# Kernel optimization log

Hardware: AMD Instinct MI355X
Metric: run time of the kernel (lower is better)

Reference implementation:

```python
import jax, jax.numpy as jnp
import numpy as np

N = 50000      # nodes
E = 800000     # edges (avg degree 16)
IN, H, C = 128, 256, 47


def _linear_init(key, nin, nout):
    bound = 1.0 / np.sqrt(nin)
    kw, kb = jax.random.split(key)
    w = jax.random.uniform(kw, (nin, nout), jnp.float32, -bound, bound)
    b = jax.random.uniform(kb, (nout,), jnp.float32, -bound, bound)
    return w, b


def setup_inputs() -> dict:
    key = jax.random.key(0)
    ks = jax.random.split(key, 9)
    x = jax.random.normal(ks[0], (N, IN), jnp.float32)
    row = jax.random.randint(ks[1], (E,), 0, N)   # dst node of each edge
    col = jax.random.randint(ks[2], (E,), 0, N)   # src node of each edge
    y = jax.random.randint(ks[3], (N,), 0, C)
    train_mask = jax.random.randint(ks[4], (N,), 0, 2).astype(jnp.bool_)
    w1n, b1n = _linear_init(ks[5], IN, H)
    w1s, b1s = _linear_init(ks[6], IN, H)
    w2n, b2n = _linear_init(ks[7], H, C)
    w2s, b2s = _linear_init(ks[8], H, C)
    return {"x": x, "row": row, "col": col, "y": y, "train_mask": train_mask,
            "w1n": w1n, "b1n": b1n, "w1s": w1s, "b1s": b1s,
            "w2n": w2n, "b2n": b2n, "w2s": w2s, "b2s": b2s}


def _mean_aggr(h, row, col):
    # sparse adjacency matmul with reduce='mean': gather src feats, scatter-mean to dst
    s = jax.ops.segment_sum(h[col], row, num_segments=N)          # [N, d]
    deg = jax.ops.segment_sum(jnp.ones((E,), h.dtype), row, num_segments=N)
    return jnp.where(deg[:, None] > 0, s / jnp.maximum(deg, 1.0)[:, None], 0.0)


def reference(x, row, col, y, train_mask,
              w1n, b1n, w1s, b1s, w2n, b2n, w2s, b2s):
    # dropout in eval mode -> identity
    h = x
    # layer 1: SAGE = linear(mean_aggr(h)) + linear(h), then ReLU
    a = _mean_aggr(h, row, col)
    h1 = jax.nn.relu((a @ w1n + b1n) + (h @ w1s + b1s))           # [N, H]
    # layer 2 (output): SAGE then log_softmax
    a2 = _mean_aggr(h1, row, col)
    logits = (a2 @ w2n + b2n) + (h1 @ w2s + b2s)                  # [N, C]
    logp = jax.nn.log_softmax(logits, axis=1)
    nll = -jnp.take_along_axis(logp, y[:, None], axis=1)[:, 0]    # [N]
    m = train_mask.astype(logits.dtype)
    # nll_loss mean over train nodes; single chunk -> loss / num_chunks == loss
    loss = jnp.sum(nll * m) / jnp.maximum(jnp.sum(m), 1.0)
    return loss
```

## Files before the change

kernel.cpp:

```cpp
#include <hip/hip_runtime.h>
#include <math.h>

#define NN 50000
#define EE 800000
#define DIN 128
#define HH 256
#define CC 47
#define LK2 264
#define GS_BLOCKS 2048
#define LOSS_BLOCKS 2048

typedef short bf16x8 __attribute__((ext_vector_type(8)));
typedef float f32x4 __attribute__((ext_vector_type(4)));
typedef float f32x2 __attribute__((ext_vector_type(2)));

static __device__ __forceinline__ unsigned short f2bf(float f) {
    unsigned u = __float_as_uint(f);
    u = u + 0x7fff + ((u >> 16) & 1);
    return (unsigned short)(u >> 16);
}

__global__ __launch_bounds__(256) void prep_kernel(
    const float* __restrict__ x, const int* __restrict__ row,
    const int* __restrict__ col, const int* __restrict__ msk,
    const float* __restrict__ w1n, const float* __restrict__ w1s,
    const float* __restrict__ b1n, const float* __restrict__ b1s,
    const float* __restrict__ w2n, const float* __restrict__ w2s,
    int* __restrict__ cnt, unsigned short* __restrict__ bucket,
    unsigned* __restrict__ xq, unsigned* __restrict__ ab,
    unsigned short* __restrict__ WB1, unsigned short* __restrict__ WB2,
    float* __restrict__ bias1, unsigned* __restrict__ znq,
    int* __restrict__ mcount, int* __restrict__ mlist)
{
    int t = blockIdx.x * 256 + threadIdx.x;
    if (t < EE) {
        int r = row[t];
        int pos = atomicAdd(&cnt[r], 1);
        if (pos < 64) bucket[r * 64 + pos] = (unsigned short)col[t];
    }
    if (t < NN) {
        *(uint4*)&znq[(size_t)t * 16 + 12] = make_uint4(0u, 0u, 0u, 0u);
        int m = msk[t] ? 1 : 0;
        unsigned long long b = __ballot(m);
        int lane = threadIdx.x & 63;
        int prefix = __popcll(b & ((1ull << lane) - 1ull));
        int tot = __popcll(b);
        int base_ = 0;
        if (lane == 0 && tot) base_ = atomicAdd(mcount, tot);
        base_ = __shfl(base_, 0);
        if (m) mlist[base_ + prefix] = t;
    }
    if (t < NN * 32) {
        int i = t >> 5, c = t & 31;
        float4 v = *(const float4*)&x[(size_t)i * DIN + c * 4];
        int p = __builtin_amdgcn_cvt_pk_fp8_f32(v.x, v.y, 0, false);
        p = __builtin_amdgcn_cvt_pk_fp8_f32(v.z, v.w, p, true);
        xq[(size_t)i * 32 + c] = (unsigned)p;
        ab[(size_t)i * 128 + 64 + 2 * c]     = (unsigned)f2bf(v.x) | ((unsigned)f2bf(v.y) << 16);
        ab[(size_t)i * 128 + 64 + 2 * c + 1] = (unsigned)f2bf(v.z) | ((unsigned)f2bf(v.w) << 16);
    }
    if (t < 65536) {
        int k = t >> 8, n = t & 255;
        float v = (k < 128) ? w1n[k * HH + n] : w1s[(k - 128) * HH + n];
        WB1[n * 256 + k] = f2bf(v);
    } else if (t < 65536 + 24576) {
        int q = t - 65536;
        int k = q / 96, n = q % 96;
        float v;
        if (n < 48) v = (n < CC) ? w2n[k * CC + n] : 0.f;
        else { int m2 = n - 48; v = (m2 < CC) ? w2s[k * CC + m2] : 0.f; }
        WB2[n * 256 + k] = f2bf(v);
    } else if (t < 65536 + 24576 + 256) {
        int n = t - 65536 - 24576;
        bias1[n] = b1n[n] + b1s[n];
    }
}

__global__ __launch_bounds__(256) void agg1(const unsigned* __restrict__ xq,
                                            const int* __restrict__ cnt,
                                            const unsigned short* __restrict__ bucket,
                                            unsigned* __restrict__ ab) {
    int wave = threadIdx.x >> 6, lane = threadIdx.x & 63;
    const int h = lane >> 5, hl = lane & 31;
    const int W = gridDim.x * 4;
    for (int i = blockIdx.x * 4 + wave; i < NN; i += W) {
        int e = cnt[i];
        float dvs = fmaxf((float)e, 1.0f);
        if (e > 64) e = 64;
        float A0=0,A1=0,A2=0,A3=0, B0=0,B1=0,B2=0,B3=0;
        float C0=0,C1=0,C2=0,C3=0, D0=0,D1=0,D2=0,D3=0;
        if (e > 0) {
            int myidx = bucket[i * 64 + min(lane, e - 1)];
            int j = 0;
            for (; j + 16 <= e; j += 16) {
                int n0 = __shfl(myidx, j + h);
                int n1 = __shfl(myidx, j + 2 + h);
                int n2 = __shfl(myidx, j + 4 + h);
                int n3 = __shfl(myidx, j + 6 + h);
                int n4 = __shfl(myidx, j + 8 + h);
                int n5 = __shfl(myidx, j + 10 + h);
                int n6 = __shfl(myidx, j + 12 + h);
                int n7 = __shfl(myidx, j + 14 + h);
                unsigned u0 = xq[(size_t)n0 * 32 + hl];
                unsigned u1 = xq[(size_t)n1 * 32 + hl];
                unsigned u2 = xq[(size_t)n2 * 32 + hl];
                unsigned u3 = xq[(size_t)n3 * 32 + hl];
                unsigned u4 = xq[(size_t)n4 * 32 + hl];
                unsigned u5 = xq[(size_t)n5 * 32 + hl];
                unsigned u6 = xq[(size_t)n6 * 32 + hl];
                unsigned u7 = xq[(size_t)n7 * 32 + hl];
                f32x2 l0 = __builtin_amdgcn_cvt_pk_f32_fp8(u0, false);
                f32x2 h0 = __builtin_amdgcn_cvt_pk_f32_fp8(u0, true);
                f32x2 l1 = __builtin_amdgcn_cvt_pk_f32_fp8(u1, false);
                f32x2 h1 = __builtin_amdgcn_cvt_pk_f32_fp8(u1, true);
                f32x2 l2 = __builtin_amdgcn_cvt_pk_f32_fp8(u2, false);
                f32x2 h2 = __builtin_amdgcn_cvt_pk_f32_fp8(u2, true);
                f32x2 l3 = __builtin_amdgcn_cvt_pk_f32_fp8(u3, false);
                f32x2 h3 = __builtin_amdgcn_cvt_pk_f32_fp8(u3, true);
                A0 += l0.x; A1 += l0.y; A2 += h0.x; A3 += h0.y;
                B0 += l1.x; B1 += l1.y; B2 += h1.x; B3 += h1.y;
                C0 += l2.x; C1 += l2.y; C2 += h2.x; C3 += h2.y;
                D0 += l3.x; D1 += l3.y; D2 += h3.x; D3 += h3.y;
                f32x2 l4 = __builtin_amdgcn_cvt_pk_f32_fp8(u4, false);
                f32x2 h4 = __builtin_amdgcn_cvt_pk_f32_fp8(u4, true);
                f32x2 l5 = __builtin_amdgcn_cvt_pk_f32_fp8(u5, false);
                f32x2 h5 = __builtin_amdgcn_cvt_pk_f32_fp8(u5, true);
                f32x2 l6 = __builtin_amdgcn_cvt_pk_f32_fp8(u6, false);
                f32x2 h6 = __builtin_amdgcn_cvt_pk_f32_fp8(u6, true);
                f32x2 l7 = __builtin_amdgcn_cvt_pk_f32_fp8(u7, false);
                f32x2 h7 = __builtin_amdgcn_cvt_pk_f32_fp8(u7, true);
                A0 += l4.x; A1 += l4.y; A2 += h4.x; A3 += h4.y;
                B0 += l5.x; B1 += l5.y; B2 += h5.x; B3 += h5.y;
                C0 += l6.x; C1 += l6.y; C2 += h6.x; C3 += h6.y;
                D0 += l7.x; D1 += l7.y; D2 += h7.x; D3 += h7.y;
            }
            for (; j + 8 <= e; j += 8) {
                int n0 = __shfl(myidx, j + h);
                int n1 = __shfl(myidx, j + 2 + h);
                int n2 = __shfl(myidx, j + 4 + h);
                int n3 = __shfl(myidx, j + 6 + h);
                unsigned u0 = xq[(size_t)n0 * 32 + hl];
                unsigned u1 = xq[(size_t)n1 * 32 + hl];
                unsigned u2 = xq[(size_t)n2 * 32 + hl];
                unsigned u3 = xq[(size_t)n3 * 32 + hl];
                f32x2 l0 = __builtin_amdgcn_cvt_pk_f32_fp8(u0, false);
                f32x2 h0 = __builtin_amdgcn_cvt_pk_f32_fp8(u0, true);
                f32x2 l1 = __builtin_amdgcn_cvt_pk_f32_fp8(u1, false);
                f32x2 h1 = __builtin_amdgcn_cvt_pk_f32_fp8(u1, true);
                f32x2 l2 = __builtin_amdgcn_cvt_pk_f32_fp8(u2, false);
                f32x2 h2 = __builtin_amdgcn_cvt_pk_f32_fp8(u2, true);
                f32x2 l3 = __builtin_amdgcn_cvt_pk_f32_fp8(u3, false);
                f32x2 h3 = __builtin_amdgcn_cvt_pk_f32_fp8(u3, true);
                A0 += l0.x; A1 += l0.y; A2 += h0.x; A3 += h0.y;
                B0 += l1.x; B1 += l1.y; B2 += h1.x; B3 += h1.y;
                C0 += l2.x; C1 += l2.y; C2 += h2.x; C3 += h2.y;
                D0 += l3.x; D1 += l3.y; D2 += h3.x; D3 += h3.y;
            }
            for (; j < e; j += 2) {
                int src = j + h;
                int n = __shfl(myidx, min(src, e - 1));
                unsigned u = xq[(size_t)n * 32 + hl];
                if (src >= e) u = 0u;
                f32x2 lo = __builtin_amdgcn_cvt_pk_f32_fp8(u, false);
                f32x2 hi = __builtin_amdgcn_cvt_pk_f32_fp8(u, true);
                A0 += lo.x; A1 += lo.y; A2 += hi.x; A3 += hi.y;
            }
        }
        float s0 = (A0 + B0) + (C0 + D0);
        float s1 = (A1 + B1) + (C1 + D1);
        float s2 = (A2 + B2) + (C2 + D2);
        float s3 = (A3 + B3) + (C3 + D3);
        s0 += __shfl_xor(s0, 32); s1 += __shfl_xor(s1, 32);
        s2 += __shfl_xor(s2, 32); s3 += __shfl_xor(s3, 32);
        if (h == 0) {
            float sc = 1.0f / dvs;
            unsigned d0 = (unsigned)f2bf(s0 * sc) | ((unsigned)f2bf(s1 * sc) << 16);
            unsigned d1 = (unsigned)f2bf(s2 * sc) | ((unsigned)f2bf(s3 * sc) << 16);
            *(uint2*)&ab[(size_t)i * 128 + 2 * hl] = make_uint2(d0, d1);
        }
    }
}

__global__ __launch_bounds__(256) void gemm12_fused(
    const unsigned short* __restrict__ AB,
    const unsigned short* __restrict__ WB1, const unsigned short* __restrict__ WB2,
    const float* __restrict__ bias1,
    const float* __restrict__ b2n, const float* __restrict__ b2s,
    unsigned* __restrict__ znq, float* __restrict__ zsb)
{
    __shared__ unsigned short sA[32 * LK2];
    __shared__ unsigned short sB[32 * LK2];
    __shared__ unsigned short sH[32 * LK2];
    const int tid = threadIdx.x;
    const int i0 = blockIdx.x * 32;
    const int wv = tid >> 6, lane = tid & 63;
    const int g = lane >> 4, l16 = lane & 15;
    const int m0 = (wv & 1) * 16, q0 = (wv >> 1) * 16;

#pragma unroll
    for (int l = 0; l < 4; ++l) {
        int c = tid + l * 256;
        int r = c >> 5, c8 = (c & 31) * 8;
        int gi = i0 + r;
        int4 v = make_int4(0, 0, 0, 0);
        if (gi < NN) v = *(const int4*)&AB[(size_t)gi * 256 + c8];
        *(int4*)&sA[r * LK2 + c8] = v;
    }

    for (int n0 = 0; n0 < 8; ++n0) {
#pragma unroll
        for (int l = 0; l < 4; ++l) {
            int c = tid + l * 256;
            int r = c >> 5, c8 = (c & 31) * 8;
            *(int4*)&sB[r * LK2 + c8] = *(const int4*)&WB1[(size_t)(n0 * 32 + r) * 256 + c8];
        }
        __syncthreads();
        f32x4 p0 = {}, p1 = {}, p2 = {}, p3 = {};
        {
            const unsigned short* ar = &sA[(m0 + l16) * LK2 + g * 8];
            const unsigned short* br = &sB[(q0 + l16) * LK2 + g * 8];
            p0 = __builtin_amdgcn_mfma_f32_16x16x32_bf16(*(const bf16x8*)(ar +   0), *(const bf16x8*)(br +   0), p0, 0, 0, 0);
            p1 = __builtin_amdgcn_mfma_f32_16x16x32_bf16(*(const bf16x8*)(ar +  32), *(const bf16x8*)(br +  32), p1, 0, 0, 0);
            p2 = __builtin_amdgcn_mfma_f32_16x16x32_bf16(*(const bf16x8*)(ar +  64), *(const bf16x8*)(br +  64), p2, 0, 0, 0);
            p3 = __builtin_amdgcn_mfma_f32_16x16x32_bf16(*(const bf16x8*)(ar +  96), *(const bf16x8*)(br +  96), p3, 0, 0, 0);
            p0 = __builtin_amdgcn_mfma_f32_16x16x32_bf16(*(const bf16x8*)(ar + 128), *(const bf16x8*)(br + 128), p0, 0, 0, 0);
            p1 = __builtin_amdgcn_mfma_f32_16x16x32_bf16(*(const bf16x8*)(ar + 160), *(const bf16x8*)(br + 160), p1, 0, 0, 0);
            p2 = __builtin_amdgcn_mfma_f32_16x16x32_bf16(*(const bf16x8*)(ar + 192), *(const bf16x8*)(br + 192), p2, 0, 0, 0);
            p3 = __builtin_amdgcn_mfma_f32_16x16x32_bf16(*(const bf16x8*)(ar + 224), *(const bf16x8*)(br + 224), p3, 0, 0, 0);
        }
        f32x4 acc = (p0 + p1) + (p2 + p3);
        int colh = n0 * 32 + q0 + l16;
        float bi = bias1[colh];
#pragma unroll
        for (int r = 0; r < 4; ++r)
            sH[(m0 + g * 4 + r) * LK2 + colh] = f2bf(fmaxf(acc[r] + bi, 0.f));
        __syncthreads();
    }

    for (int m = 0; m < 3; ++m) {
#pragma unroll
        for (int l = 0; l < 4; ++l) {
            int c = tid + l * 256;
            int r = c >> 5, c8 = (c & 31) * 8;
            *(int4*)&sB[r * LK2 + c8] = *(const int4*)&WB2[(size_t)(m * 32 + r) * 256 + c8];
        }
        __syncthreads();
        f32x4 p0 = {}, p1 = {}, p2 = {}, p3 = {};
        {
            const unsigned short* ar = &sH[(m0 + l16) * LK2 + g * 8];
            const unsigned short* br = &sB[(q0 + l16) * LK2 + g * 8];
            p0 = __builtin_amdgcn_mfma_f32_16x16x32_bf16(*(const bf16x8*)(ar +   0), *(const bf16x8*)(br +   0), p0, 0, 0, 0);
            p1 = __builtin_amdgcn_mfma_f32_16x16x32_bf16(*(const bf16x8*)(ar +  32), *(const bf16x8*)(br +  32), p1, 0, 0, 0);
            p2 = __builtin_amdgcn_mfma_f32_16x16x32_bf16(*(const bf16x8*)(ar +  64), *(const bf16x8*)(br +  64), p2, 0, 0, 0);
            p3 = __builtin_amdgcn_mfma_f32_16x16x32_bf16(*(const bf16x8*)(ar +  96), *(const bf16x8*)(br +  96), p3, 0, 0, 0);
            p0 = __builtin_amdgcn_mfma_f32_16x16x32_bf16(*(const bf16x8*)(ar + 128), *(const bf16x8*)(br + 128), p0, 0, 0, 0);
            p1 = __builtin_amdgcn_mfma_f32_16x16x32_bf16(*(const bf16x8*)(ar + 160), *(const bf16x8*)(br + 160), p1, 0, 0, 0);
            p2 = __builtin_amdgcn_mfma_f32_16x16x32_bf16(*(const bf16x8*)(ar + 192), *(const bf16x8*)(br + 192), p2, 0, 0, 0);
            p3 = __builtin_amdgcn_mfma_f32_16x16x32_bf16(*(const bf16x8*)(ar + 224), *(const bf16x8*)(br + 224), p3, 0, 0, 0);
        }
        f32x4 acc = (p0 + p1) + (p2 + p3);
        int c = m * 32 + q0 + l16;
        if (c < 48) {
#pragma unroll
            for (int r = 0; r < 4; ++r) {
                int gi = i0 + m0 + g * 4 + r;
                float v = acc[r];
                float v1 = __shfl_down(v, 1);
                float v2 = __shfl_down(v, 2);
                float v3 = __shfl_down(v, 3);
                if (((l16 & 3) == 0) && gi < NN) {
                    int pk = __builtin_amdgcn_cvt_pk_fp8_f32(v, v1, 0, false);
                    pk = __builtin_amdgcn_cvt_pk_fp8_f32(v2, v3, pk, true);
                    znq[(size_t)gi * 16 + (c >> 2)] = (unsigned)pk;
                }
            }
        } else {
            int cz = c - 48;
            float bias = (cz < CC) ? (b2n[cz] + b2s[cz]) : 0.f;
#pragma unroll
            for (int r = 0; r < 4; ++r) {
                int gi = i0 + m0 + g * 4 + r;
                if (gi < NN) zsb[(size_t)gi * 48 + cz] = acc[r] + bias;
            }
        }
        __syncthreads();
    }
}

__global__ __launch_bounds__(256) void loss_kernel(
    const unsigned* __restrict__ znq, const float* __restrict__ zsb,
    const int* __restrict__ cnt, const unsigned short* __restrict__ bucket,
    const int* __restrict__ y, const int* __restrict__ mcount,
    const int* __restrict__ mlist, float* __restrict__ partials)
{
    __shared__ float red[16];
    const int tid = threadIdx.x;
    const int wave = tid >> 6, lane = tid & 63;
    const int half = lane >> 5, hl = lane & 31;
    const int h32 = lane & 32;
    const int eg = hl >> 4, dwl = hl & 15;
    const int HW = gridDim.x * 8;
    const int M = mcount[0];
    float num = 0.f, den = 0.f;

    for (int pa = ((blockIdx.x * 4 + wave) * 2 + half) * 2; pa < M; pa += 2 * HW) {
        int i0 = mlist[pa];
        bool v1 = (pa + 1 < M);
        int i1 = v1 ? mlist[pa + 1] : i0;
        int c0 = cnt[i0], c1 = cnt[i1];
        int e0 = min(c0, 64), e1 = min(c1, 64);
        int yi0 = y[i0], yi1 = y[i1];
        int mi0 = bucket[(size_t)i0 * 64 + min(hl, max(e0 - 1, 0))];
        int mi1 = bucket[(size_t)i1 * 64 + min(hl, max(e1 - 1, 0))];
        int dwm = min(dwl, 11);
        float4 zs0 = *(const float4*)&zsb[(size_t)i0 * 48 + 4 * dwm];
        float4 zs1 = *(const float4*)&zsb[(size_t)i1 * 48 + 4 * dwm];

        unsigned ua[16], ub[16];
#pragma unroll
        for (int q = 0; q < 16; ++q) {
            int n = __shfl(mi0, h32 + 2 * q + eg);
            ua[q] = znq[(size_t)n * 16 + dwl];
        }
#pragma unroll
        for (int q = 0; q < 16; ++q) {
            int n = __shfl(mi1, h32 + 2 * q + eg);
            ub[q] = znq[(size_t)n * 16 + dwl];
        }
        float a0=0.f,a1=0.f,a2=0.f,a3=0.f, b0=0.f,b1=0.f,b2=0.f,b3=0.f;
#pragma unroll
        for (int q = 0; q < 16; ++q) {
            int s = 2 * q + eg;
            unsigned u = (s < e0) ? ua[q] : 0u;
            f32x2 lo = __builtin_amdgcn_cvt_pk_f32_fp8(u, false);
            f32x2 hi = __builtin_amdgcn_cvt_pk_f32_fp8(u, true);
            a0 += lo.x; a1 += lo.y; a2 += hi.x; a3 += hi.y;
            unsigned w = (s < e1) ? ub[q] : 0u;
            f32x2 lo2 = __builtin_amdgcn_cvt_pk_f32_fp8(w, false);
            f32x2 hi2 = __builtin_amdgcn_cvt_pk_f32_fp8(w, true);
            b0 += lo2.x; b1 += lo2.y; b2 += hi2.x; b3 += hi2.y;
        }
        if (e0 > 32 || e1 > 32) {
            int mj0 = bucket[(size_t)i0 * 64 + min(32 + hl, max(e0 - 1, 0))];
            int mj1 = bucket[(size_t)i1 * 64 + min(32 + hl, max(e1 - 1, 0))];
            unsigned va[16], vb[16];
#pragma unroll
            for (int q = 0; q < 16; ++q) {
                int n = __shfl(mj0, h32 + 2 * q + eg);
                va[q] = znq[(size_t)n * 16 + dwl];
            }
#pragma unroll
            for (int q = 0; q < 16; ++q) {
                int n = __shfl(mj1, h32 + 2 * q + eg);
                vb[q] = znq[(size_t)n * 16 + dwl];
            }
#pragma unroll
            for (int q = 0; q < 16; ++q) {
                int s = 32 + 2 * q + eg;
                unsigned u = (s < e0) ? va[q] : 0u;
                f32x2 lo = __builtin_amdgcn_cvt_pk_f32_fp8(u, false);
                f32x2 hi = __builtin_amdgcn_cvt_pk_f32_fp8(u, true);
                a0 += lo.x; a1 += lo.y; a2 += hi.x; a3 += hi.y;
                unsigned w = (s < e1) ? vb[q] : 0u;
                f32x2 lo2 = __builtin_amdgcn_cvt_pk_f32_fp8(w, false);
                f32x2 hi2 = __builtin_amdgcn_cvt_pk_f32_fp8(w, true);
                b0 += lo2.x; b1 += lo2.y; b2 += hi2.x; b3 += hi2.y;
            }
        }
        a0 += __shfl_xor(a0, 16); a1 += __shfl_xor(a1, 16);
        a2 += __shfl_xor(a2, 16); a3 += __shfl_xor(a3, 16);
        b0 += __shfl_xor(b0, 16); b1 += __shfl_xor(b1, 16);
        b2 += __shfl_xor(b2, 16); b3 += __shfl_xor(b3, 16);

        float sc0 = 1.0f / fmaxf((float)c0, 1.0f);
        float sc1 = 1.0f / fmaxf((float)c1, 1.0f);
        float l0=-1e30f,l1=-1e30f,l2=-1e30f,l3=-1e30f;
        float m0=-1e30f,m1=-1e30f,m2=-1e30f,m3=-1e30f;
        if (dwl < 12) {
            l0 = a0 * sc0 + zs0.x;
            l1 = a1 * sc0 + zs0.y;
            l2 = a2 * sc0 + zs0.z;
            l3 = (dwl == 11) ? -1e30f : (a3 * sc0 + zs0.w);
            m0 = b0 * sc1 + zs1.x;
            m1 = b1 * sc1 + zs1.y;
            m2 = b2 * sc1 + zs1.z;
            m3 = (dwl == 11) ? -1e30f : (b3 * sc1 + zs1.w);
        }
        float mx0 = fmaxf(fmaxf(l0, l1), fmaxf(l2, l3));
        float mx1 = fmaxf(fmaxf(m0, m1), fmaxf(m2, m3));
#pragma unroll
        for (int off = 8; off >= 1; off >>= 1) {
            mx0 = fmaxf(mx0, __shfl_xor(mx0, off));
            mx1 = fmaxf(mx1, __shfl_xor(mx1, off));
        }
        float s0 = __expf(l0 - mx0) + __expf(l1 - mx0) +
                   __expf(l2 - mx0) + __expf(l3 - mx0);
        float s1 = __expf(m0 - mx1) + __expf(m1 - mx1) +
                   __expf(m2 - mx1) + __expf(m3 - mx1);
#pragma unroll
        for (int off = 8; off >= 1; off >>= 1) {
            s0 += __shfl_xor(s0, off);
            s1 += __shfl_xor(s1, off);
        }
        float lse0 = mx0 + __logf(s0);
        float lse1 = mx1 + __logf(s1);

        float va0 = (yi0 & 2) ? ((yi0 & 1) ? l3 : l2) : ((yi0 & 1) ? l1 : l0);
        float ly0 = __shfl(va0, h32 + (yi0 >> 2));
        float vb0 = (yi1 & 2) ? ((yi1 & 1) ? m3 : m2) : ((yi1 & 1) ? m1 : m0);
        float ly1 = __shfl(vb0, h32 + (yi1 >> 2));
        if (hl == 0) {
            num += (lse0 - ly0) + (v1 ? (lse1 - ly1) : 0.f);
            den += 1.f + (v1 ? 1.f : 0.f);
        }
    }

    if (hl == 0) {
        red[wave * 4 + half * 2]     = num;
        red[wave * 4 + half * 2 + 1] = den;
    }
    __syncthreads();
    if (tid == 0) {
        float n = 0.f, d = 0.f;
#pragma unroll
        for (int k = 0; k < 16; k += 2) { n += red[k]; d += red[k + 1]; }
        *(float2*)&partials[2 * blockIdx.x] = make_float2(n, d);
    }
}

__global__ __launch_bounds__(256) void finalize_kernel(
    const float* __restrict__ partials, float* __restrict__ out)
{
    __shared__ float sn[4], sd[4];
    int tid = threadIdx.x;
    float n = 0.f, d = 0.f;
    for (int i = tid; i < LOSS_BLOCKS; i += 256) {
        float2 p = *(const float2*)&partials[2 * i];
        n += p.x; d += p.y;
    }
#pragma unroll
    for (int off = 32; off >= 1; off >>= 1) {
        n += __shfl_xor(n, off);
        d += __shfl_xor(d, off);
    }
    int wv = tid >> 6;
    if ((tid & 63) == 0) { sn[wv] = n; sd[wv] = d; }
    __syncthreads();
    if (tid == 0) {
        float N = (sn[0] + sn[1]) + (sn[2] + sn[3]);
        float D = (sd[0] + sd[1]) + (sd[2] + sd[3]);
        out[0] = N / fmaxf(D, 1.0f);
    }
}

extern "C" void kernel_launch(void* const* d_in, const int* in_sizes, int n_in,
                              void* d_out, int out_size, void* d_ws, size_t ws_size,
                              hipStream_t stream) {
    const float* x   = (const float*)d_in[0];
    const int*   row = (const int*)d_in[1];
    const int*   col = (const int*)d_in[2];
    const int*   y   = (const int*)d_in[3];
    const int*   msk = (const int*)d_in[4];
    const float* w1n = (const float*)d_in[5];
    const float* b1n = (const float*)d_in[6];
    const float* w1s = (const float*)d_in[7];
    const float* b1s = (const float*)d_in[8];
    const float* w2n = (const float*)d_in[9];
    const float* b2n = (const float*)d_in[10];
    const float* w2s = (const float*)d_in[11];
    const float* b2s = (const float*)d_in[12];
    float* out = (float*)d_out;

    float* ws       = (float*)d_ws;
    float* partials = ws;
    int*   mcount   = (int*)(ws + 2 * LOSS_BLOCKS);
    int*   cnt      = (int*)(ws + 2 * LOSS_BLOCKS + 32);
    unsigned short* bucket = (unsigned short*)(cnt + 50048);
    unsigned* xq   = (unsigned*)(bucket + 3200000);
    unsigned* ab   = xq + (size_t)NN * 32;
    unsigned* znq  = ab + (size_t)NN * 128;
    float* zsb     = (float*)(znq + (size_t)NN * 16);
    unsigned short* WB1 = (unsigned short*)(zsb + (size_t)NN * 48);
    unsigned short* WB2 = WB1 + 65536;
    float* bias1   = (float*)(WB2 + 24576);
    int*   mlist   = (int*)(bias1 + 256);

    (void)hipMemsetAsync(mcount, 0, (32 + 50048) * sizeof(int), stream);

    prep_kernel<<<(NN * 32 + 255) / 256, 256, 0, stream>>>(
        x, row, col, msk, w1n, w1s, b1n, b1s, w2n, w2s,
        cnt, bucket, xq, ab, WB1, WB2, bias1, znq, mcount, mlist);

    agg1<<<GS_BLOCKS, 256, 0, stream>>>(xq, cnt, bucket, ab);

    gemm12_fused<<<(NN + 31) / 32, 256, 0, stream>>>(
        (const unsigned short*)ab, WB1, WB2, bias1, b2n, b2s, znq, zsb);

    loss_kernel<<<LOSS_BLOCKS, 256, 0, stream>>>(
        znq, zsb, cnt, bucket, y, mcount, mlist, partials);

    finalize_kernel<<<1, 256, 0, stream>>>(partials, out);
}
```

Before: 215.1 us.

## Fuse layer-1 mean aggregation into the fused GEMM kernel's shared-memory A tile

```diff
diff --git a/kernel.cpp b/kernel.cpp
--- a/kernel.cpp
+++ b/kernel.cpp
@@ -7,7 +7,6 @@
 #define HH 256
 #define CC 47
 #define LK2 264
-#define GS_BLOCKS 2048
 #define LOSS_BLOCKS 2048
 
 typedef short bf16x8 __attribute__((ext_vector_type(8)));
@@ -27,7 +26,7 @@
     const float* __restrict__ b1n, const float* __restrict__ b1s,
     const float* __restrict__ w2n, const float* __restrict__ w2s,
     int* __restrict__ cnt, unsigned short* __restrict__ bucket,
-    unsigned* __restrict__ xq, unsigned* __restrict__ ab,
+    unsigned* __restrict__ xq, unsigned* __restrict__ xb,
     unsigned short* __restrict__ WB1, unsigned short* __restrict__ WB2,
     float* __restrict__ bias1, unsigned* __restrict__ znq,
     int* __restrict__ mcount, int* __restrict__ mlist)
@@ -36,7 +35,8 @@
     if (t < EE) {
         int r = row[t];
         int pos = atomicAdd(&cnt[r], 1);
-        if (pos < 64) bucket[r * 64 + pos] = (unsigned short)col[t];
+        if (pos < 64)
+            __builtin_nontemporal_store((unsigned short)col[t], &bucket[r * 64 + pos]);
     }
     if (t < NN) {
         *(uint4*)&znq[(size_t)t * 16 + 12] = make_uint4(0u, 0u, 0u, 0u);
@@ -56,8 +56,8 @@
         int p = __builtin_amdgcn_cvt_pk_fp8_f32(v.x, v.y, 0, false);
         p = __builtin_amdgcn_cvt_pk_fp8_f32(v.z, v.w, p, true);
         xq[(size_t)i * 32 + c] = (unsigned)p;
-        ab[(size_t)i * 128 + 64 + 2 * c]     = (unsigned)f2bf(v.x) | ((unsigned)f2bf(v.y) << 16);
-        ab[(size_t)i * 128 + 64 + 2 * c + 1] = (unsigned)f2bf(v.z) | ((unsigned)f2bf(v.w) << 16);
+        xb[(size_t)i * 64 + 2 * c]     = (unsigned)f2bf(v.x) | ((unsigned)f2bf(v.y) << 16);
+        xb[(size_t)i * 64 + 2 * c + 1] = (unsigned)f2bf(v.z) | ((unsigned)f2bf(v.w) << 16);
     }
     if (t < 65536) {
         int k = t >> 8, n = t & 255;
@@ -76,113 +76,10 @@
     }
 }
 
-__global__ __launch_bounds__(256) void agg1(const unsigned* __restrict__ xq,
-                                            const int* __restrict__ cnt,
-                                            const unsigned short* __restrict__ bucket,
-                                            unsigned* __restrict__ ab) {
-    int wave = threadIdx.x >> 6, lane = threadIdx.x & 63;
-    const int h = lane >> 5, hl = lane & 31;
-    const int W = gridDim.x * 4;
-    for (int i = blockIdx.x * 4 + wave; i < NN; i += W) {
-        int e = cnt[i];
-        float dvs = fmaxf((float)e, 1.0f);
-        if (e > 64) e = 64;
-        float A0=0,A1=0,A2=0,A3=0, B0=0,B1=0,B2=0,B3=0;
-        float C0=0,C1=0,C2=0,C3=0, D0=0,D1=0,D2=0,D3=0;
-        if (e > 0) {
-            int myidx = bucket[i * 64 + min(lane, e - 1)];
-            int j = 0;
-            for (; j + 16 <= e; j += 16) {
-                int n0 = __shfl(myidx, j + h);
-                int n1 = __shfl(myidx, j + 2 + h);
-                int n2 = __shfl(myidx, j + 4 + h);
-                int n3 = __shfl(myidx, j + 6 + h);
-                int n4 = __shfl(myidx, j + 8 + h);
-                int n5 = __shfl(myidx, j + 10 + h);
-                int n6 = __shfl(myidx, j + 12 + h);
-                int n7 = __shfl(myidx, j + 14 + h);
-                unsigned u0 = xq[(size_t)n0 * 32 + hl];
-                unsigned u1 = xq[(size_t)n1 * 32 + hl];
-                unsigned u2 = xq[(size_t)n2 * 32 + hl];
-                unsigned u3 = xq[(size_t)n3 * 32 + hl];
-                unsigned u4 = xq[(size_t)n4 * 32 + hl];
-                unsigned u5 = xq[(size_t)n5 * 32 + hl];
-                unsigned u6 = xq[(size_t)n6 * 32 + hl];
-                unsigned u7 = xq[(size_t)n7 * 32 + hl];
-                f32x2 l0 = __builtin_amdgcn_cvt_pk_f32_fp8(u0, false);
-                f32x2 h0 = __builtin_amdgcn_cvt_pk_f32_fp8(u0, true);
-                f32x2 l1 = __builtin_amdgcn_cvt_pk_f32_fp8(u1, false);
-                f32x2 h1 = __builtin_amdgcn_cvt_pk_f32_fp8(u1, true);
-                f32x2 l2 = __builtin_amdgcn_cvt_pk_f32_fp8(u2, false);
-                f32x2 h2 = __builtin_amdgcn_cvt_pk_f32_fp8(u2, true);
-                f32x2 l3 = __builtin_amdgcn_cvt_pk_f32_fp8(u3, false);
-                f32x2 h3 = __builtin_amdgcn_cvt_pk_f32_fp8(u3, true);
-                A0 += l0.x; A1 += l0.y; A2 += h0.x; A3 += h0.y;
-                B0 += l1.x; B1 += l1.y; B2 += h1.x; B3 += h1.y;
-                C0 += l2.x; C1 += l2.y; C2 += h2.x; C3 += h2.y;
-                D0 += l3.x; D1 += l3.y; D2 += h3.x; D3 += h3.y;
-                f32x2 l4 = __builtin_amdgcn_cvt_pk_f32_fp8(u4, false);
-                f32x2 h4 = __builtin_amdgcn_cvt_pk_f32_fp8(u4, true);
-                f32x2 l5 = __builtin_amdgcn_cvt_pk_f32_fp8(u5, false);
-                f32x2 h5 = __builtin_amdgcn_cvt_pk_f32_fp8(u5, true);
-                f32x2 l6 = __builtin_amdgcn_cvt_pk_f32_fp8(u6, false);
-                f32x2 h6 = __builtin_amdgcn_cvt_pk_f32_fp8(u6, true);
-                f32x2 l7 = __builtin_amdgcn_cvt_pk_f32_fp8(u7, false);
-                f32x2 h7 = __builtin_amdgcn_cvt_pk_f32_fp8(u7, true);
-                A0 += l4.x; A1 += l4.y; A2 += h4.x; A3 += h4.y;
-                B0 += l5.x; B1 += l5.y; B2 += h5.x; B3 += h5.y;
-                C0 += l6.x; C1 += l6.y; C2 += h6.x; C3 += h6.y;
-                D0 += l7.x; D1 += l7.y; D2 += h7.x; D3 += h7.y;
-            }
-            for (; j + 8 <= e; j += 8) {
-                int n0 = __shfl(myidx, j + h);
-                int n1 = __shfl(myidx, j + 2 + h);
-                int n2 = __shfl(myidx, j + 4 + h);
-                int n3 = __shfl(myidx, j + 6 + h);
-                unsigned u0 = xq[(size_t)n0 * 32 + hl];
-                unsigned u1 = xq[(size_t)n1 * 32 + hl];
-                unsigned u2 = xq[(size_t)n2 * 32 + hl];
-                unsigned u3 = xq[(size_t)n3 * 32 + hl];
-                f32x2 l0 = __builtin_amdgcn_cvt_pk_f32_fp8(u0, false);
-                f32x2 h0 = __builtin_amdgcn_cvt_pk_f32_fp8(u0, true);
-                f32x2 l1 = __builtin_amdgcn_cvt_pk_f32_fp8(u1, false);
-                f32x2 h1 = __builtin_amdgcn_cvt_pk_f32_fp8(u1, true);
-                f32x2 l2 = __builtin_amdgcn_cvt_pk_f32_fp8(u2, false);
-                f32x2 h2 = __builtin_amdgcn_cvt_pk_f32_fp8(u2, true);
-                f32x2 l3 = __builtin_amdgcn_cvt_pk_f32_fp8(u3, false);
-                f32x2 h3 = __builtin_amdgcn_cvt_pk_f32_fp8(u3, true);
-                A0 += l0.x; A1 += l0.y; A2 += h0.x; A3 += h0.y;
-                B0 += l1.x; B1 += l1.y; B2 += h1.x; B3 += h1.y;
-                C0 += l2.x; C1 += l2.y; C2 += h2.x; C3 += h2.y;
-                D0 += l3.x; D1 += l3.y; D2 += h3.x; D3 += h3.y;
-            }
-            for (; j < e; j += 2) {
-                int src = j + h;
-                int n = __shfl(myidx, min(src, e - 1));
-                unsigned u = xq[(size_t)n * 32 + hl];
-                if (src >= e) u = 0u;
-                f32x2 lo = __builtin_amdgcn_cvt_pk_f32_fp8(u, false);
-                f32x2 hi = __builtin_amdgcn_cvt_pk_f32_fp8(u, true);
-                A0 += lo.x; A1 += lo.y; A2 += hi.x; A3 += hi.y;
-            }
-        }
-        float s0 = (A0 + B0) + (C0 + D0);
-        float s1 = (A1 + B1) + (C1 + D1);
-        float s2 = (A2 + B2) + (C2 + D2);
-        float s3 = (A3 + B3) + (C3 + D3);
-        s0 += __shfl_xor(s0, 32); s1 += __shfl_xor(s1, 32);
-        s2 += __shfl_xor(s2, 32); s3 += __shfl_xor(s3, 32);
-        if (h == 0) {
-            float sc = 1.0f / dvs;
-            unsigned d0 = (unsigned)f2bf(s0 * sc) | ((unsigned)f2bf(s1 * sc) << 16);
-            unsigned d1 = (unsigned)f2bf(s2 * sc) | ((unsigned)f2bf(s3 * sc) << 16);
-            *(uint2*)&ab[(size_t)i * 128 + 2 * hl] = make_uint2(d0, d1);
-        }
-    }
-}
-
 __global__ __launch_bounds__(256) void gemm12_fused(
-    const unsigned short* __restrict__ AB,
+    const unsigned* __restrict__ xq, const int* __restrict__ cnt,
+    const unsigned short* __restrict__ bucket,
+    const unsigned short* __restrict__ XB,
     const unsigned short* __restrict__ WB1, const unsigned short* __restrict__ WB2,
     const float* __restrict__ bias1,
     const float* __restrict__ b2n, const float* __restrict__ b2s,
@@ -196,15 +93,120 @@
     const int wv = tid >> 6, lane = tid & 63;
     const int g = lane >> 4, l16 = lane & 15;
     const int m0 = (wv & 1) * 16, q0 = (wv >> 1) * 16;
-
-#pragma unroll
-    for (int l = 0; l < 4; ++l) {
+    const int h = lane >> 5, hl = lane & 31;
+
+#pragma unroll
+    for (int l = 0; l < 2; ++l) {
         int c = tid + l * 256;
-        int r = c >> 5, c8 = (c & 31) * 8;
+        int r = c >> 4, c8 = (c & 15) * 8;
         int gi = i0 + r;
         int4 v = make_int4(0, 0, 0, 0);
-        if (gi < NN) v = *(const int4*)&AB[(size_t)gi * 256 + c8];
-        *(int4*)&sA[r * LK2 + c8] = v;
+        if (gi < NN) v = *(const int4*)&XB[(size_t)gi * 128 + c8];
+        *(int4*)&sA[r * LK2 + 128 + c8] = v;
+    }
+
+    {
+        int c8v = 0;
+        int gi8 = i0 + (wv << 3) + hl;
+        if (hl < 8 && gi8 < NN) c8v = cnt[gi8];
+        for (int rr = 0; rr < 8; ++rr) {
+            int r = (wv << 3) + rr;
+            int gi = i0 + r;
+            int e = __shfl(c8v, rr);
+            float dvs = fmaxf((float)e, 1.0f);
+            if (e > 64) e = 64;
+            float A0=0,A1=0,A2=0,A3=0, B0=0,B1=0,B2=0,B3=0;
+            float C0=0,C1=0,C2=0,C3=0, D0=0,D1=0,D2=0,D3=0;
+            if (e > 0) {
+                int myidx = bucket[gi * 64 + min(lane, e - 1)];
+                int j = 0;
+                for (; j + 16 <= e; j += 16) {
+                    int n0 = __shfl(myidx, j + h);
+                    int n1 = __shfl(myidx, j + 2 + h);
+                    int n2 = __shfl(myidx, j + 4 + h);
+                    int n3 = __shfl(myidx, j + 6 + h);
+                    int n4 = __shfl(myidx, j + 8 + h);
+                    int n5 = __shfl(myidx, j + 10 + h);
+                    int n6 = __shfl(myidx, j + 12 + h);
+                    int n7 = __shfl(myidx, j + 14 + h);
+                    unsigned u0 = xq[(size_t)n0 * 32 + hl];
+                    unsigned u1 = xq[(size_t)n1 * 32 + hl];
+                    unsigned u2 = xq[(size_t)n2 * 32 + hl];
+                    unsigned u3 = xq[(size_t)n3 * 32 + hl];
+                    unsigned u4 = xq[(size_t)n4 * 32 + hl];
+                    unsigned u5 = xq[(size_t)n5 * 32 + hl];
+                    unsigned u6 = xq[(size_t)n6 * 32 + hl];
+                    unsigned u7 = xq[(size_t)n7 * 32 + hl];
+                    f32x2 l0 = __builtin_amdgcn_cvt_pk_f32_fp8(u0, false);
+                    f32x2 h0 = __builtin_amdgcn_cvt_pk_f32_fp8(u0, true);
+                    f32x2 l1 = __builtin_amdgcn_cvt_pk_f32_fp8(u1, false);
+                    f32x2 h1 = __builtin_amdgcn_cvt_pk_f32_fp8(u1, true);
+                    f32x2 l2 = __builtin_amdgcn_cvt_pk_f32_fp8(u2, false);
+                    f32x2 h2 = __builtin_amdgcn_cvt_pk_f32_fp8(u2, true);
+                    f32x2 l3 = __builtin_amdgcn_cvt_pk_f32_fp8(u3, false);
+                    f32x2 h3 = __builtin_amdgcn_cvt_pk_f32_fp8(u3, true);
+                    A0 += l0.x; A1 += l0.y; A2 += h0.x; A3 += h0.y;
+                    B0 += l1.x; B1 += l1.y; B2 += h1.x; B3 += h1.y;
+                    C0 += l2.x; C1 += l2.y; C2 += h2.x; C3 += h2.y;
+                    D0 += l3.x; D1 += l3.y; D2 += h3.x; D3 += h3.y;
+                    f32x2 l4 = __builtin_amdgcn_cvt_pk_f32_fp8(u4, false);
+                    f32x2 h4 = __builtin_amdgcn_cvt_pk_f32_fp8(u4, true);
+                    f32x2 l5 = __builtin_amdgcn_cvt_pk_f32_fp8(u5, false);
+                    f32x2 h5 = __builtin_amdgcn_cvt_pk_f32_fp8(u5, true);
+                    f32x2 l6 = __builtin_amdgcn_cvt_pk_f32_fp8(u6, false);
+                    f32x2 h6 = __builtin_amdgcn_cvt_pk_f32_fp8(u6, true);
+                    f32x2 l7 = __builtin_amdgcn_cvt_pk_f32_fp8(u7, false);
+                    f32x2 h7 = __builtin_amdgcn_cvt_pk_f32_fp8(u7, true);
+                    A0 += l4.x; A1 += l4.y; A2 += h4.x; A3 += h4.y;
+                    B0 += l5.x; B1 += l5.y; B2 += h5.x; B3 += h5.y;
+                    C0 += l6.x; C1 += l6.y; C2 += h6.x; C3 += h6.y;
+                    D0 += l7.x; D1 += l7.y; D2 += h7.x; D3 += h7.y;
+                }
+                for (; j + 8 <= e; j += 8) {
+                    int n0 = __shfl(myidx, j + h);
+                    int n1 = __shfl(myidx, j + 2 + h);
+                    int n2 = __shfl(myidx, j + 4 + h);
+                    int n3 = __shfl(myidx, j + 6 + h);
+                    unsigned u0 = xq[(size_t)n0 * 32 + hl];
+                    unsigned u1 = xq[(size_t)n1 * 32 + hl];
+                    unsigned u2 = xq[(size_t)n2 * 32 + hl];
+                    unsigned u3 = xq[(size_t)n3 * 32 + hl];
+                    f32x2 l0 = __builtin_amdgcn_cvt_pk_f32_fp8(u0, false);
+                    f32x2 h0 = __builtin_amdgcn_cvt_pk_f32_fp8(u0, true);
+                    f32x2 l1 = __builtin_amdgcn_cvt_pk_f32_fp8(u1, false);
+                    f32x2 h1 = __builtin_amdgcn_cvt_pk_f32_fp8(u1, true);
+                    f32x2 l2 = __builtin_amdgcn_cvt_pk_f32_fp8(u2, false);
+                    f32x2 h2 = __builtin_amdgcn_cvt_pk_f32_fp8(u2, true);
+                    f32x2 l3 = __builtin_amdgcn_cvt_pk_f32_fp8(u3, false);
+                    f32x2 h3 = __builtin_amdgcn_cvt_pk_f32_fp8(u3, true);
+                    A0 += l0.x; A1 += l0.y; A2 += h0.x; A3 += h0.y;
+                    B0 += l1.x; B1 += l1.y; B2 += h1.x; B3 += h1.y;
+                    C0 += l2.x; C1 += l2.y; C2 += h2.x; C3 += h2.y;
+                    D0 += l3.x; D1 += l3.y; D2 += h3.x; D3 += h3.y;
+                }
+                for (; j < e; j += 2) {
+                    int src = j + h;
+                    int n = __shfl(myidx, min(src, e - 1));
+                    unsigned u = xq[(size_t)n * 32 + hl];
+                    if (src >= e) u = 0u;
+                    f32x2 lo = __builtin_amdgcn_cvt_pk_f32_fp8(u, false);
+                    f32x2 hi = __builtin_amdgcn_cvt_pk_f32_fp8(u, true);
+                    A0 += lo.x; A1 += lo.y; A2 += hi.x; A3 += hi.y;
+                }
+            }
+            float s0 = (A0 + B0) + (C0 + D0);
+            float s1 = (A1 + B1) + (C1 + D1);
+            float s2 = (A2 + B2) + (C2 + D2);
+            float s3 = (A3 + B3) + (C3 + D3);
+            s0 += __shfl_xor(s0, 32); s1 += __shfl_xor(s1, 32);
+            s2 += __shfl_xor(s2, 32); s3 += __shfl_xor(s3, 32);
+            if (h == 0) {
+                float sc = 1.0f / dvs;
+                unsigned d0 = (unsigned)f2bf(s0 * sc) | ((unsigned)f2bf(s1 * sc) << 16);
+                unsigned d1 = (unsigned)f2bf(s2 * sc) | ((unsigned)f2bf(s3 * sc) << 16);
+                *(uint2*)&sA[r * LK2 + 4 * hl] = make_uint2(d0, d1);
+            }
+        }
     }
 
     for (int n0 = 0; n0 < 8; ++n0) {
@@ -477,8 +479,8 @@
     int*   cnt      = (int*)(ws + 2 * LOSS_BLOCKS + 32);
     unsigned short* bucket = (unsigned short*)(cnt + 50048);
     unsigned* xq   = (unsigned*)(bucket + 3200000);
-    unsigned* ab   = xq + (size_t)NN * 32;
-    unsigned* znq  = ab + (size_t)NN * 128;
+    unsigned* xb   = xq + (size_t)NN * 32;
+    unsigned* znq  = xb + (size_t)NN * 64;
     float* zsb     = (float*)(znq + (size_t)NN * 16);
     unsigned short* WB1 = (unsigned short*)(zsb + (size_t)NN * 48);
     unsigned short* WB2 = WB1 + 65536;
@@ -489,12 +491,11 @@
 
     prep_kernel<<<(NN * 32 + 255) / 256, 256, 0, stream>>>(
         x, row, col, msk, w1n, w1s, b1n, b1s, w2n, w2s,
-        cnt, bucket, xq, ab, WB1, WB2, bias1, znq, mcount, mlist);
-
-    agg1<<<GS_BLOCKS, 256, 0, stream>>>(xq, cnt, bucket, ab);
+        cnt, bucket, xq, xb, WB1, WB2, bias1, znq, mcount, mlist);
 
     gemm12_fused<<<(NN + 31) / 32, 256, 0, stream>>>(
-        (const unsigned short*)ab, WB1, WB2, bias1, b2n, b2s, znq, zsb);
+        xq, cnt, bucket, (const unsigned short*)xb,
+        WB1, WB2, bias1, b2n, b2s, znq, zsb);
 
     loss_kernel<<<LOSS_BLOCKS, 256, 0, stream>>>(
         znq, zsb, cnt, bucket, y, mcount, mlist, partials);
```

Measured after the change: 242.2 us. 1.13x slower.
